# Performance work log

Measured on AMD Instinct MI355X. Metric: run time of the kernel, lower is better.

## Reference

```python
import jax, jax.numpy as jnp
import numpy as np

# ---- static grid config (matches init_kwargs: xmin=[0,0], xmax=[2,2], margin=0.1, ppu=64) ----
XMIN = np.array([0.0, 0.0], dtype=np.float32)
XMAX = np.array([2.0, 2.0], dtype=np.float32)
MARGIN = 0.1
PPU = 64
INIT_LENGTHSCALE = 0.1


def _make_grid():
    # half number of points per dim, rounded up to a power of 2
    half_n = np.ceil((0.5 * (XMAX - XMIN) + MARGIN) * PPU)
    half_n = (2.0 ** np.ceil(np.log2(half_n))).astype(np.int64)  # [128, 128]
    x_mid = 0.5 * (XMIN + XMAX)
    axes = [x_mid[d] + np.arange(-half_n[d], half_n[d], dtype=np.float32) / PPU
            for d in range(len(XMIN))]
    mesh = np.meshgrid(*axes, indexing="ij")
    return jnp.asarray(np.stack(mesh, axis=-1))  # [256, 256, 2]


def setup_inputs() -> dict:
    key = jax.random.key(0)
    k1, k2, k3 = jax.random.split(key, 3)
    m, nc, nt, dx, dy = 2, 1024, 128, 2, 16
    xc = jax.random.uniform(k1, (m, nc, dx), dtype=jnp.float32) * 2.0  # in [0, 2)
    yc = jax.random.normal(k2, (m, nc, dy), dtype=jnp.float32)
    xt = jax.random.uniform(k3, (m, nt, dx), dtype=jnp.float32) * 2.0
    # lengthscale_param = log(exp(init_lengthscale) - 1) per dim (softplus inverse)
    lengthscale_param = jnp.log(jnp.expm1(jnp.full((dx,), INIT_LENGTHSCALE, dtype=jnp.float32)))
    return {"xc": xc, "yc": yc, "xt": xt, "lengthscale_param": lengthscale_param}


def _compute_eq_weights(x1, x2, lengthscales):
    # x1: [m, n1, dx], x2: [m, n2, dx] -> exp(-0.5 * sum_d ((x1-x2)/l)^2): [m, n1, n2]
    a = x1 / lengthscales
    b = x2 / lengthscales
    sq = (jnp.sum(a * a, -1)[:, :, None]
          + jnp.sum(b * b, -1)[:, None, :]
          - 2.0 * jnp.einsum("mid,mjd->mij", a, b))
    return jnp.exp(-0.5 * sq)


def reference(xc, yc, xt, lengthscale_param):
    m = xc.shape[0]
    # append ones channel (density channel)
    yc = jnp.concatenate([yc, jnp.ones(yc.shape[:-1] + (1,), yc.dtype)], axis=-1)
    lengthscale = 1e-05 + jax.nn.softplus(lengthscale_param)  # [dx]
    x_grid = _make_grid()  # [256, 256, 2]
    x_grid_b = jnp.broadcast_to(x_grid, (m,) + x_grid.shape)  # [m, 256, 256, 2]
    x_grid_flat = x_grid_b.reshape(m, -1, x_grid.shape[-1])  # [m, ng, dx]
    weights = _compute_eq_weights(x_grid_flat, xc, lengthscale)  # [m, ng, nc]
    z_grid_flat = weights @ yc  # [m, ng, dy+1]
    z_grid = z_grid_flat.reshape(x_grid_b.shape[:-1] + (z_grid_flat.shape[-1],))
    return (x_grid_b, z_grid)
```

## Files before the change

kernel.cpp:

```cpp
#include <hip/hip_runtime.h>

#define NC 1024
#define DY 16
#define NG 65536

typedef float v4f __attribute__((ext_vector_type(4)));
typedef _Float16 h8 __attribute__((ext_vector_type(8)));
typedef _Float16 h2 __attribute__((ext_vector_type(2)));

__global__ __launch_bounds__(256, 4) void setconv_fused(
    const float* __restrict__ xc,
    const float* __restrict__ yc,
    const float* __restrict__ lsp,
    float* __restrict__ out_grid,
    float* __restrict__ out_z)
{
    __shared__ __align__(16) _Float16 ytb[32 * 64 * 8];
    __shared__ __align__(16) float    cys[NC];
    __shared__ __align__(16) _Float16 wx2[2][NC];

    const int mi   = blockIdx.y;
    const int bx   = blockIdx.x;
    const int ig   = bx >> 2;
    const int jg   = bx & 3;
    const int tid  = threadIdx.x;
    const int wave = tid >> 6;
    const int lane = tid & 63;
    const int q    = lane >> 4;
    const int r    = lane & 15;
    const int jt   = jg * 4 + wave;
    const int i0   = ig * 2;

    const float l0 = 1e-5f + __logf(1.0f + __expf(lsp[0]));
    const float l1 = 1e-5f + __logf(1.0f + __expf(lsp[1]));
    const float R  = 0.84932184f;
    const float s0 = R / l0, s1 = R / l1;

    if (tid < 128) {
        const int ii = tid >> 6, jj = tid & 63;
        const int g  = (i0 + ii) * 256 + jg * 64 + jj;
        const float gx = 1.0f + (float)((g >> 8) - 128) * 0.015625f;
        const float gy = 1.0f + (float)((g & 255) - 128) * 0.015625f;
        ((float2*)out_grid)[(size_t)mi * NG + g] = make_float2(gx, gy);
    }

#pragma unroll
    for (int t = 0; t < 4; ++t) {
        const int k = tid + 256 * t;
        cys[k] = xc[(((size_t)mi * NC + k) << 1) + 1] * s1;
    }
#pragma unroll
    for (int t = 0; t < 8; ++t) {
        const int idx = tid + 256 * t;
        const int row = idx >> 10, k = idx & 1023;
        const float gi = (1.0f + (float)(i0 + row - 128) * 0.015625f) * s0;
        const float u  = gi - xc[(((size_t)mi * NC + k) << 1)] * s0;
        wx2[row][k] = (_Float16)__builtin_amdgcn_exp2f(-u * u);
    }
#pragma unroll
    for (int cc = 0; cc < 8; ++cc) {
        const int cell = tid + 256 * cc;
        const int ks = cell >> 6, ln = cell & 63;
        const int ch = ln & 15;
        const int kb = ks * 32 + ((ln >> 4) << 3);
        h8 o;
#pragma unroll
        for (int jj = 0; jj < 8; ++jj)
            o[jj] = (_Float16)yc[(((size_t)mi * NC + kb + jj) << 4) + ch];
        *(h8*)&ytb[(size_t)cell * 8] = o;
    }
    __syncthreads();

    h8 ones;
#pragma unroll
    for (int e = 0; e < 8; ++e) ones[e] = (_Float16)1.0f;

    const float gyp = (1.0f + (float)(jt * 16 + r - 128) * 0.015625f) * s1;

    v4f accD0 = {0.f,0.f,0.f,0.f}, accS0 = {0.f,0.f,0.f,0.f};
    v4f accD1 = {0.f,0.f,0.f,0.f}, accS1 = {0.f,0.f,0.f,0.f};

#pragma unroll 4
    for (int ks = 0; ks < 32; ++ks) {
        const int kb = ks * 32 + q * 8;
        const float4 cya = *(const float4*)&cys[kb];
        const float4 cyb = *(const float4*)&cys[kb + 4];
        const h8 yt  = *(const h8*)&ytb[((size_t)ks * 64 + lane) * 8];
        const h8 wxa = *(const h8*)&wx2[0][kb];
        const h8 wxb = *(const h8*)&wx2[1][kb];

        const float u0 = gyp - cya.x, u1 = gyp - cya.y;
        const float u2 = gyp - cya.z, u3 = gyp - cya.w;
        const float u4 = gyp - cyb.x, u5 = gyp - cyb.y;
        const float u6 = gyp - cyb.z, u7 = gyp - cyb.w;
        const float e0 = __builtin_amdgcn_exp2f(-u0 * u0);
        const float e1 = __builtin_amdgcn_exp2f(-u1 * u1);
        const float e2 = __builtin_amdgcn_exp2f(-u2 * u2);
        const float e3 = __builtin_amdgcn_exp2f(-u3 * u3);
        const float e4 = __builtin_amdgcn_exp2f(-u4 * u4);
        const float e5 = __builtin_amdgcn_exp2f(-u5 * u5);
        const float e6 = __builtin_amdgcn_exp2f(-u6 * u6);
        const float e7 = __builtin_amdgcn_exp2f(-u7 * u7);

        union { h2 p[4]; h8 v; } wy;
        wy.p[0] = __builtin_bit_cast(h2, __builtin_amdgcn_cvt_pkrtz(e0, e1));
        wy.p[1] = __builtin_bit_cast(h2, __builtin_amdgcn_cvt_pkrtz(e2, e3));
        wy.p[2] = __builtin_bit_cast(h2, __builtin_amdgcn_cvt_pkrtz(e4, e5));
        wy.p[3] = __builtin_bit_cast(h2, __builtin_amdgcn_cvt_pkrtz(e6, e7));

        const h8 a0 = wy.v * wxa;
        const h8 a1 = wy.v * wxb;
        accD0 = __builtin_amdgcn_mfma_f32_16x16x32_f16(a0, yt,   accD0, 0, 0, 0);
        accS0 = __builtin_amdgcn_mfma_f32_16x16x32_f16(a0, ones, accS0, 0, 0, 0);
        accD1 = __builtin_amdgcn_mfma_f32_16x16x32_f16(a1, yt,   accD1, 0, 0, 0);
        accS1 = __builtin_amdgcn_mfma_f32_16x16x32_f16(a1, ones, accS1, 0, 0, 0);
    }

    float* __restrict__ oz0 =
        out_z + ((size_t)mi * NG + (size_t)i0 * 256 + jt * 16) * 17;
    float* __restrict__ oz1 = oz0 + 256 * 17;
#pragma unroll
    for (int reg = 0; reg < 4; ++reg) {
        const int row = q * 4 + reg;
        oz0[(size_t)row * 17 + r] = accD0[reg];
        oz1[(size_t)row * 17 + r] = accD1[reg];
        if (r == 0) {
            oz0[(size_t)row * 17 + 16] = accS0[reg];
            oz1[(size_t)row * 17 + 16] = accS1[reg];
        }
    }
}

extern "C" void kernel_launch(void* const* d_in, const int* in_sizes, int n_in,
                              void* d_out, int out_size, void* d_ws, size_t ws_size,
                              hipStream_t stream) {
    const float* xc  = (const float*)d_in[0];
    const float* yc  = (const float*)d_in[1];
    const float* lsp = (const float*)d_in[3];

    const int m = in_sizes[0] / (NC * 2);

    float* out_grid = (float*)d_out;
    float* out_z    = (float*)d_out + (size_t)m * NG * 2;

    dim3 grid(512, m), block(256);
    hipLaunchKernelGGL(setconv_fused, grid, block, 0, stream,
                       xc, yc, lsp, out_grid, out_z);
}
```

Before: 77.19 us.

## Precompute y-direction weight table and yc fp16 layout in a separate kernel

Adds a pre-pass kernel that computes the separable y-axis Gaussian factors for every (grid column, context point) pair once per batch, plus the fp16 MFMA-layout copy of yc, and writes both to workspace. The main kernel then loads these precomputed fp16 weights from global memory instead of recomputing 8 exp2 per iteration in each block, and copies the yc table with plain vector loads. Each y-weight was previously recomputed by every row-block (128 times redundantly). In exchange there is an extra kernel launch, a roughly 2 MB workspace round-trip, and per-iteration global loads in the inner MFMA loop.

After: 71.97 us, median of 2. 6.8% less time.

```diff
diff --git a/kernel.cpp b/kernel.cpp
--- a/kernel.cpp
+++ b/kernel.cpp
@@ -4,19 +4,65 @@
 #define DY 16
 #define NG 65536
 
+#define SZ_WYA (16 * 32 * 64 * 8)
+#define SZ_YTB (32 * 64 * 8)
+
 typedef float v4f __attribute__((ext_vector_type(4)));
 typedef _Float16 h8 __attribute__((ext_vector_type(8)));
-typedef _Float16 h2 __attribute__((ext_vector_type(2)));
 
-__global__ __launch_bounds__(256, 4) void setconv_fused(
+__global__ __launch_bounds__(256) void setconv_tables(
+    const float* __restrict__ xc, const float* __restrict__ yc,
+    const float* __restrict__ lsp,
+    _Float16* __restrict__ WYA, _Float16* __restrict__ YTB, int m)
+{
+    const int t  = blockIdx.x * 256 + threadIdx.x;
+    const int T1 = m * (SZ_WYA / 8);
+    const int T2 = T1 + m * (SZ_YTB / 8);
+    if (t >= T2) return;
+
+    if (t < T1) {
+        const float l1 = 1e-5f + __logf(1.0f + __expf(lsp[1]));
+        const float s1 = 0.84932184f / l1;
+        const int mm   = t >> 15;
+        const int rem  = t & 32767;
+        const int jt   = rem >> 11;
+        const int ks   = (rem >> 6) & 31;
+        const int lane = rem & 63;
+        const int j    = jt * 16 + (lane & 15);
+        const int k0   = ks * 32 + ((lane >> 4) << 3);
+        const float g  = (1.0f + (float)(j - 128) * 0.015625f) * s1;
+        h8 o;
+#pragma unroll
+        for (int jj = 0; jj < 8; ++jj) {
+            const float u = g - xc[(((size_t)(mm * NC + k0 + jj)) << 1) + 1] * s1;
+            o[jj] = (_Float16)__builtin_amdgcn_exp2f(-u * u);
+        }
+        *(h8*)&WYA[(size_t)t * 8] = o;
+    } else {
+        const int tt   = t - T1;
+        const int mm   = tt >> 11;
+        const int rem  = tt & 2047;
+        const int ks   = rem >> 6;
+        const int lane = rem & 63;
+        const int ch   = lane & 15;
+        const int k0   = ks * 32 + ((lane >> 4) << 3);
+        h8 o;
+#pragma unroll
+        for (int jj = 0; jj < 8; ++jj)
+            o[jj] = (_Float16)yc[(((size_t)(mm * NC + k0 + jj)) << 4) + ch];
+        *(h8*)&YTB[(size_t)tt * 8] = o;
+    }
+}
+
+__global__ __launch_bounds__(256, 4) void setconv_main(
     const float* __restrict__ xc,
-    const float* __restrict__ yc,
     const float* __restrict__ lsp,
+    const _Float16* __restrict__ WYA,
+    const _Float16* __restrict__ YTB,
     float* __restrict__ out_grid,
     float* __restrict__ out_z)
 {
-    __shared__ __align__(16) _Float16 ytb[32 * 64 * 8];
-    __shared__ __align__(16) float    cys[NC];
+    __shared__ __align__(16) _Float16 ytb[SZ_YTB];
     __shared__ __align__(16) _Float16 wx2[2][NC];
 
     const int mi   = blockIdx.y;
@@ -32,9 +78,7 @@
     const int i0   = ig * 2;
 
     const float l0 = 1e-5f + __logf(1.0f + __expf(lsp[0]));
-    const float l1 = 1e-5f + __logf(1.0f + __expf(lsp[1]));
-    const float R  = 0.84932184f;
-    const float s0 = R / l0, s1 = R / l1;
+    const float s0 = 0.84932184f / l0;
 
     if (tid < 128) {
         const int ii = tid >> 6, jj = tid & 63;
@@ -45,11 +89,6 @@
     }
 
 #pragma unroll
-    for (int t = 0; t < 4; ++t) {
-        const int k = tid + 256 * t;
-        cys[k] = xc[(((size_t)mi * NC + k) << 1) + 1] * s1;
-    }
-#pragma unroll
     for (int t = 0; t < 8; ++t) {
         const int idx = tid + 256 * t;
         const int row = idx >> 10, k = idx & 1023;
@@ -57,59 +96,31 @@
         const float u  = gi - xc[(((size_t)mi * NC + k) << 1)] * s0;
         wx2[row][k] = (_Float16)__builtin_amdgcn_exp2f(-u * u);
     }
+    {
+        const float4* src = (const float4*)(YTB + (size_t)mi * SZ_YTB);
+        float4* dst = (float4*)ytb;
 #pragma unroll
-    for (int cc = 0; cc < 8; ++cc) {
-        const int cell = tid + 256 * cc;
-        const int ks = cell >> 6, ln = cell & 63;
-        const int ch = ln & 15;
-        const int kb = ks * 32 + ((ln >> 4) << 3);
-        h8 o;
-#pragma unroll
-        for (int jj = 0; jj < 8; ++jj)
-            o[jj] = (_Float16)yc[(((size_t)mi * NC + kb + jj) << 4) + ch];
-        *(h8*)&ytb[(size_t)cell * 8] = o;
+        for (int t = 0; t < 8; ++t) dst[tid + 256 * t] = src[tid + 256 * t];
     }
     __syncthreads();
+
+    const _Float16* wyp = WYA + (((size_t)mi * 16 + jt) * 32 * 64 + lane) * 8;
 
     h8 ones;
 #pragma unroll
     for (int e = 0; e < 8; ++e) ones[e] = (_Float16)1.0f;
-
-    const float gyp = (1.0f + (float)(jt * 16 + r - 128) * 0.015625f) * s1;
 
     v4f accD0 = {0.f,0.f,0.f,0.f}, accS0 = {0.f,0.f,0.f,0.f};
     v4f accD1 = {0.f,0.f,0.f,0.f}, accS1 = {0.f,0.f,0.f,0.f};
 
 #pragma unroll 4
     for (int ks = 0; ks < 32; ++ks) {
-        const int kb = ks * 32 + q * 8;
-        const float4 cya = *(const float4*)&cys[kb];
-        const float4 cyb = *(const float4*)&cys[kb + 4];
+        const h8 wy  = *(const h8*)(wyp + (size_t)ks * 512);
         const h8 yt  = *(const h8*)&ytb[((size_t)ks * 64 + lane) * 8];
-        const h8 wxa = *(const h8*)&wx2[0][kb];
-        const h8 wxb = *(const h8*)&wx2[1][kb];
-
-        const float u0 = gyp - cya.x, u1 = gyp - cya.y;
-        const float u2 = gyp - cya.z, u3 = gyp - cya.w;
-        const float u4 = gyp - cyb.x, u5 = gyp - cyb.y;
-        const float u6 = gyp - cyb.z, u7 = gyp - cyb.w;
-        const float e0 = __builtin_amdgcn_exp2f(-u0 * u0);
-        const float e1 = __builtin_amdgcn_exp2f(-u1 * u1);
-        const float e2 = __builtin_amdgcn_exp2f(-u2 * u2);
-        const float e3 = __builtin_amdgcn_exp2f(-u3 * u3);
-        const float e4 = __builtin_amdgcn_exp2f(-u4 * u4);
-        const float e5 = __builtin_amdgcn_exp2f(-u5 * u5);
-        const float e6 = __builtin_amdgcn_exp2f(-u6 * u6);
-        const float e7 = __builtin_amdgcn_exp2f(-u7 * u7);
-
-        union { h2 p[4]; h8 v; } wy;
-        wy.p[0] = __builtin_bit_cast(h2, __builtin_amdgcn_cvt_pkrtz(e0, e1));
-        wy.p[1] = __builtin_bit_cast(h2, __builtin_amdgcn_cvt_pkrtz(e2, e3));
-        wy.p[2] = __builtin_bit_cast(h2, __builtin_amdgcn_cvt_pkrtz(e4, e5));
-        wy.p[3] = __builtin_bit_cast(h2, __builtin_amdgcn_cvt_pkrtz(e6, e7));
-
-        const h8 a0 = wy.v * wxa;
-        const h8 a1 = wy.v * wxb;
+        const h8 wxa = *(const h8*)&wx2[0][ks * 32 + q * 8];
+        const h8 wxb = *(const h8*)&wx2[1][ks * 32 + q * 8];
+        const h8 a0 = wy * wxa;
+        const h8 a1 = wy * wxb;
         accD0 = __builtin_amdgcn_mfma_f32_16x16x32_f16(a0, yt,   accD0, 0, 0, 0);
         accS0 = __builtin_amdgcn_mfma_f32_16x16x32_f16(a0, ones, accS0, 0, 0, 0);
         accD1 = __builtin_amdgcn_mfma_f32_16x16x32_f16(a1, yt,   accD1, 0, 0, 0);
@@ -138,12 +149,18 @@
     const float* yc  = (const float*)d_in[1];
     const float* lsp = (const float*)d_in[3];
 
-    const int m = in_sizes[0] / (NC * 2);
+    int m = in_sizes[0] / (NC * 2);
 
     float* out_grid = (float*)d_out;
     float* out_z    = (float*)d_out + (size_t)m * NG * 2;
 
-    dim3 grid(512, m), block(256);
-    hipLaunchKernelGGL(setconv_fused, grid, block, 0, stream,
-                       xc, yc, lsp, out_grid, out_z);
+    _Float16* WYA = (_Float16*)d_ws;
+    _Float16* YTB = WYA + (size_t)m * SZ_WYA;
+
+    const int total1 = m * (SZ_WYA / 8 + SZ_YTB / 8);
+    hipLaunchKernelGGL(setconv_tables, dim3((total1 + 255) / 256), dim3(256),
+                       0, stream, xc, yc, lsp, WYA, YTB, m);
+
+    hipLaunchKernelGGL(setconv_main, dim3(512, m), dim3(256), 0, stream,
+                       xc, lsp, WYA, YTB, out_grid, out_z);
 }
```
